# Kernel optimization log

Hardware: AMD Instinct MI355X
Metric: run time of the kernel (lower is better)

## Reference

```python
import jax, jax.numpy as jnp
import numpy as np

N, E, D_IN, D_OUT = 100000, 640000, 128, 128


def setup_inputs() -> dict:
    key = jax.random.key(0)
    ks = jax.random.split(key, 8)
    x = jax.random.normal(ks[0], (N, D_IN), dtype=jnp.float32)
    edge_index = jax.random.randint(ks[1], (2, E), 0, N, dtype=jnp.int64)
    s = 1.0 / np.sqrt(D_IN)
    W_lin = jax.random.uniform(ks[2], (D_IN, D_OUT), jnp.float32, -s, s)
    b_lin = jax.random.uniform(ks[3], (D_OUT,), jnp.float32, -s, s)
    W_st = jax.random.uniform(ks[4], (D_IN, D_OUT), jnp.float32, -s, s)
    b_st = jax.random.uniform(ks[5], (D_OUT,), jnp.float32, -s, s)
    W_ts = jax.random.uniform(ks[6], (D_IN, D_OUT), jnp.float32, -s, s)
    b_ts = jax.random.uniform(ks[7], (D_OUT,), jnp.float32, -s, s)
    return {"x": x, "edge_index": edge_index, "W_lin": W_lin, "b_lin": b_lin,
            "W_st": W_st, "b_st": b_st, "W_ts": W_ts, "b_ts": b_ts}


def _scatter_mean(feat_src, idx_dst, num_nodes):
    # gather-then-segment-sum mean aggregation over variable-degree neighborhoods
    summed = jax.ops.segment_sum(feat_src, idx_dst, num_segments=num_nodes)
    cnt = jax.ops.segment_sum(jnp.ones((feat_src.shape[0],), feat_src.dtype),
                              idx_dst, num_segments=num_nodes)
    return summed / jnp.maximum(cnt, 1.0)[:, None]


def reference(x, edge_index, W_lin, b_lin, W_st, b_st, W_ts, b_ts):
    src, dst = edge_index[0], edge_index[1]
    alpha = 0.5
    # SAGEConv(flow='source_to_target', root_weight=False): mean over in-neighbors (src -> dst)
    agg_st = _scatter_mean(x[src], dst, x.shape[0])
    out_st = agg_st @ W_st + b_st
    # SAGEConv(flow='target_to_source'): mean over out-neighbors (dst -> src)
    agg_ts = _scatter_mean(x[dst], src, x.shape[0])
    out_ts = agg_ts @ W_ts + b_ts
    return x @ W_lin + b_lin + (1.0 - alpha) * out_st + alpha * out_ts
```

## Files before the change

### kernel.cpp

```cpp
#include <hip/hip_runtime.h>

#define D    128
#define BROW 32
#define CAPE 31

typedef short short8 __attribute__((ext_vector_type(8)));
typedef float f32x4  __attribute__((ext_vector_type(4)));

static __device__ __forceinline__ unsigned short f2bf(float f) {
    union { float f; unsigned u; } v; v.f = f;
    unsigned r = v.u + 0x7FFFu + ((v.u >> 16) & 1u);
    return (unsigned short)(r >> 16);
}
static __device__ __forceinline__ float bf2f(unsigned short h) {
    union { unsigned u; float f; } v; v.u = ((unsigned)h) << 16;
    return v.f;
}

#define CH 2048

__global__ __launch_bounds__(256) void k_phase0(
    const float* __restrict__ x, const int* __restrict__ ei,
    const float* __restrict__ W_lin, const float* __restrict__ W_st,
    const float* __restrict__ W_ts,
    unsigned short* __restrict__ xb, unsigned short* __restrict__ wtf,
    int* __restrict__ cnt, int* __restrict__ ent,
    int E, int N, int t8, int nbuild, int ncvt)
{
    int b = blockIdx.x;
    if (b < nbuild) {
        const int part  = b & 7;
        const int chunk = b >> 3;
        const int P  = (2 * N + 7) >> 3;
        const int lo = part * P;
        const int hi = lo + P;
        int gg[16], vv[16], pp[16];
        #pragma unroll
        for (int k = 0; k < 8; ++k) {
            int e = chunk * CH + k * 256 + threadIdx.x;
            int s = -1, d = -1;
            if (e < E) { s = ei[e]; d = ei[E + e]; }
            int gts = N + s;
            gg[2 * k]     = (s >= 0 && d >= lo && d < hi) ? d : -1;
            vv[2 * k]     = s;
            gg[2 * k + 1] = (s >= 0 && gts >= lo && gts < hi) ? gts : -1;
            vv[2 * k + 1] = d;
        }
        #pragma unroll
        for (int k = 0; k < 16; ++k)
            if (gg[k] >= 0) pp[k] = atomicAdd(cnt + gg[k], 1);
        #pragma unroll
        for (int k = 0; k < 16; ++k)
            if (gg[k] >= 0 && pp[k] < CAPE)
                ent[(size_t)gg[k] * BROW + pp[k]] = vv[k];
    } else if (b < nbuild + ncvt) {
        int i = (b - nbuild) * 256 + threadIdx.x;
        if (i >= t8) return;
        const float4* p = (const float4*)(x + (size_t)i * 8);
        float4 a = p[0], c = p[1];
        unsigned r0 = (unsigned)f2bf(a.x) | ((unsigned)f2bf(a.y) << 16);
        unsigned r1 = (unsigned)f2bf(a.z) | ((unsigned)f2bf(a.w) << 16);
        unsigned r2 = (unsigned)f2bf(c.x) | ((unsigned)f2bf(c.y) << 16);
        unsigned r3 = (unsigned)f2bf(c.z) | ((unsigned)f2bf(c.w) << 16);
        *((uint4*)(xb + (size_t)i * 8)) = make_uint4(r0, r1, r2, r3);
    } else {
        int g = (b - nbuild - ncvt) * 256 + threadIdx.x;
        if (g >= 3 * 4 * 8 * 64) return;
        int lane = g & 63;
        int tile = (g >> 6) & 7;
        int ks   = (g >> 9) & 3;
        int m    = g >> 11;
        const float* W = (m == 0) ? W_lin : (m == 1) ? W_st : W_ts;
        float scale = (m == 0) ? 1.0f : 0.5f;
        int n = tile * 16 + (lane & 15);
        int kbase = ks * 32 + (lane >> 4) * 8;
        unsigned short* dst = wtf + (size_t)g * 8;
        #pragma unroll
        for (int j = 0; j < 8; ++j)
            dst[j] = f2bf(W[(size_t)(kbase + j) * D + n] * scale);
    }
}

__global__ __launch_bounds__(256, 5) void k_fused(
    const unsigned short* __restrict__ xb,
    const int* __restrict__ cnt, const int* __restrict__ ent,
    const unsigned short* __restrict__ wtf,
    const float* __restrict__ b_lin, const float* __restrict__ b_st,
    const float* __restrict__ b_ts,
    float* __restrict__ out, int N)
{
    __shared__ unsigned short aggF[2 * 4 * 64 * 4 * 8];

    const int tid  = threadIdx.x;
    const int row0 = blockIdx.x * 64;

    {
        const int grp = tid >> 3;
        const int l8  = tid & 7;
        const int ks  = l8 >> 1;
        const int qd0 = (l8 & 1) * 2;
        const unsigned short* xcol = xb + (l8 << 4);

        int slot0 = grp * 4;
        int gn = row0 + (slot0 & 63); if (gn > N - 1) gn = N - 1;
        size_t g = (size_t)(slot0 >> 6) * N + gn;
        const int* row = ent + g * BROW;
        int4 h = *(const int4*)row;
        int dg = cnt[g];

        for (int s = 0; s < 4; ++s) {
            const int* rowN = row; int4 hn = h; int dgn = dg;
            if (s < 3) {
                int slot1 = grp * 4 + s + 1;
                int gn1 = row0 + (slot1 & 63); if (gn1 > N - 1) gn1 = N - 1;
                size_t g1 = (size_t)(slot1 >> 6) * N + gn1;
                rowN = ent + g1 * BROW;
                hn = *(const int4*)rowN;
                dgn = cnt[g1];
            }
            int slotc = grp * 4 + s;
            int dirc = slotc >> 6, ic = slotc & 63;
            int deg = dg > CAPE ? CAPE : dg;

            float a0[8], a1[8];
            #pragma unroll
            for (int t = 0; t < 8; ++t) { a0[t] = 0.f; a1[t] = 0.f; }

            int j = 0;
            if (deg >= 4) {
                {
                    const unsigned short* r0 = xcol + (size_t)h.x * D;
                    const unsigned short* r1 = xcol + (size_t)h.y * D;
                    const unsigned short* r2 = xcol + (size_t)h.z * D;
                    const unsigned short* r3 = xcol + (size_t)h.w * D;
                    short8 u00 = *(const short8*)r0, u01 = *(const short8*)(r0 + 8);
                    short8 u10 = *(const short8*)r1, u11 = *(const short8*)(r1 + 8);
                    short8 u20 = *(const short8*)r2, u21 = *(const short8*)(r2 + 8);
                    short8 u30 = *(const short8*)r3, u31 = *(const short8*)(r3 + 8);
                    #pragma unroll
                    for (int t = 0; t < 8; ++t) {
                        a0[t] += (bf2f((unsigned short)u00[t]) + bf2f((unsigned short)u10[t]))
                               + (bf2f((unsigned short)u20[t]) + bf2f((unsigned short)u30[t]));
                        a1[t] += (bf2f((unsigned short)u01[t]) + bf2f((unsigned short)u11[t]))
                               + (bf2f((unsigned short)u21[t]) + bf2f((unsigned short)u31[t]));
                    }
                }
                for (j = 4; j + 4 <= deg; j += 4) {
                    const unsigned short* r0 = xcol + (size_t)row[j]     * D;
                    const unsigned short* r1 = xcol + (size_t)row[j + 1] * D;
                    const unsigned short* r2 = xcol + (size_t)row[j + 2] * D;
                    const unsigned short* r3 = xcol + (size_t)row[j + 3] * D;
                    short8 u00 = *(const short8*)r0, u01 = *(const short8*)(r0 + 8);
                    short8 u10 = *(const short8*)r1, u11 = *(const short8*)(r1 + 8);
                    short8 u20 = *(const short8*)r2, u21 = *(const short8*)(r2 + 8);
                    short8 u30 = *(const short8*)r3, u31 = *(const short8*)(r3 + 8);
                    #pragma unroll
                    for (int t = 0; t < 8; ++t) {
                        a0[t] += (bf2f((unsigned short)u00[t]) + bf2f((unsigned short)u10[t]))
                               + (bf2f((unsigned short)u20[t]) + bf2f((unsigned short)u30[t]));
                        a1[t] += (bf2f((unsigned short)u01[t]) + bf2f((unsigned short)u11[t]))
                               + (bf2f((unsigned short)u21[t]) + bf2f((unsigned short)u31[t]));
                    }
                }
            }
            for (; j < deg; ++j) {
                const unsigned short* r = xcol + (size_t)row[j] * D;
                short8 u0 = *(const short8*)r, u1 = *(const short8*)(r + 8);
                #pragma unroll
                for (int t = 0; t < 8; ++t) {
                    a0[t] += bf2f((unsigned short)u0[t]);
                    a1[t] += bf2f((unsigned short)u1[t]);
                }
            }

            float inv = 1.0f / fmaxf((float)deg, 1.0f);
            short8 o0, o1;
            #pragma unroll
            for (int t = 0; t < 8; ++t) {
                o0[t] = (short)f2bf(a0[t] * inv);
                o1[t] = (short)f2bf(a1[t] * inv);
            }
            short8* afp = ((short8*)aggF) + (((dirc * 4 + ks) * 64 + ic) * 4) + qd0;
            afp[0] = o0;
            afp[1] = o1;

            row = rowN; h = hn; dg = dgn;
        }
    }

    const int w    = tid >> 6;
    const int lane = tid & 63;
    const int quad = lane >> 4;
    const int l15  = lane & 15;
    const int wrow = w * 16 + l15;
    int rowA = row0 + wrow; if (rowA > N - 1) rowA = N - 1;

    f32x4 acc[8];
    #pragma unroll
    for (int t = 0; t < 8; ++t) acc[t] = (f32x4){0.f, 0.f, 0.f, 0.f};

    {
        short8 a[4];
        const unsigned short* ap = xb + (size_t)rowA * D + quad * 8;
        #pragma unroll
        for (int ks = 0; ks < 4; ++ks)
            a[ks] = *(const short8*)(ap + ks * 32);
        const short8* bw = (const short8*)wtf;
        #pragma unroll
        for (int ks = 0; ks < 4; ++ks) {
            #pragma unroll
            for (int t = 0; t < 8; ++t) {
                short8 bb = bw[(ks * 8 + t) * 64 + lane];
                acc[t] = __builtin_amdgcn_mfma_f32_16x16x32_bf16(a[ks], bb, acc[t], 0, 0, 0);
            }
        }
    }
    __syncthreads();

    for (int m = 1; m < 3; ++m) {
        short8 a[4];
        const short8* af = (const short8*)aggF;
        #pragma unroll
        for (int ks = 0; ks < 4; ++ks)
            a[ks] = af[(((m - 1) * 4 + ks) << 8) + wrow * 4 + quad];
        const short8* bw = ((const short8*)wtf) + m * 2048;
        #pragma unroll
        for (int ks = 0; ks < 4; ++ks) {
            #pragma unroll
            for (int t = 0; t < 8; ++t) {
                short8 bb = bw[(ks * 8 + t) * 64 + lane];
                acc[t] = __builtin_amdgcn_mfma_f32_16x16x32_bf16(a[ks], bb, acc[t], 0, 0, 0);
            }
        }
    }

    #pragma unroll
    for (int t = 0; t < 8; ++t) {
        int col = t * 16 + l15;
        float bj = b_lin[col] + 0.5f * (b_st[col] + b_ts[col]);
        #pragma unroll
        for (int i = 0; i < 4; ++i) {
            int row = row0 + w * 16 + quad * 4 + i;
            if (row < N)
                __builtin_nontemporal_store(acc[t][i] + bj, &out[(size_t)row * D + col]);
        }
    }
}

extern "C" void kernel_launch(void* const* d_in, const int* in_sizes, int n_in,
                              void* d_out, int out_size, void* d_ws, size_t ws_size,
                              hipStream_t stream)
{
    const float* x     = (const float*)d_in[0];
    const int*   ei    = (const int*)d_in[1];
    const float* W_lin = (const float*)d_in[2];
    const float* b_lin = (const float*)d_in[3];
    const float* W_st  = (const float*)d_in[4];
    const float* b_st  = (const float*)d_in[5];
    const float* W_ts  = (const float*)d_in[6];
    const float* b_ts  = (const float*)d_in[7];
    float*       out   = (float*)d_out;

    const int N = in_sizes[0] / D;
    const int E = in_sizes[1] / 2;
    const int M = 2 * N;

    char* base = (char*)d_ws;
    int* cnt             = (int*)base;            base += (size_t)M * 4;
    int* ent             = (int*)base;            base += (size_t)M * BROW * 4;
    unsigned short* xb   = (unsigned short*)base; base += (size_t)N * D * 2;
    unsigned short* wtf  = (unsigned short*)base; base += 3 * 16384 * 2;

    hipMemsetAsync(cnt, 0, (size_t)M * 4, stream);

    const int t8     = N * D / 8;
    const int nbuild = 8 * ((E + CH - 1) / CH);
    const int ncvt   = (t8 + 255) / 256;
    const int nprep  = 24;

    k_phase0<<<dim3(nbuild + ncvt + nprep), dim3(256), 0, stream>>>(
        x, ei, W_lin, W_st, W_ts, xb, wtf, cnt, ent, E, N, t8, nbuild, ncvt);
    k_fused<<<dim3((N + 63) / 64), dim3(256), 0, stream>>>(
        xb, cnt, ent, wtf, b_lin, b_st, b_ts, out, N);
}
```

Measured before the change: 269.4 us.

## Halve rows per block, widen gather lanes, pad with zero row

Each block now covers 32 rows instead of 64, so the grid doubles and occupancy is raised to 6 waves per SIMD. The gather gives each of 16 lanes 8 columns per neighbor, in place of 8 lanes with 16 columns, and the final MFMA stage is split so each wave computes 4 of the 8 column tiles. A zero row appended to the bf16 copy of x lets the gather loop always fetch four neighbors per step, padding with that row, which removes the scalar remainder loop and branch divergence. The cost is more redundant loads of the weight fragments per block and some wasted loads on the zero row.

```diff
diff --git a/kernel.cpp b/kernel.cpp
--- a/kernel.cpp
+++ b/kernel.cpp
@@ -55,7 +55,11 @@
                 ent[(size_t)gg[k] * BROW + pp[k]] = vv[k];
     } else if (b < nbuild + ncvt) {
         int i = (b - nbuild) * 256 + threadIdx.x;
-        if (i >= t8) return;
+        if (i >= t8 + D / 8) return;
+        if (i >= t8) {
+            *((uint4*)(xb + (size_t)i * 8)) = make_uint4(0, 0, 0, 0);
+            return;
+        }
         const float4* p = (const float4*)(x + (size_t)i * 8);
         float4 a = p[0], c = p[1];
         unsigned r0 = (unsigned)f2bf(a.x) | ((unsigned)f2bf(a.y) << 16);
@@ -81,7 +85,7 @@
     }
 }
 
-__global__ __launch_bounds__(256, 5) void k_fused(
+__global__ __launch_bounds__(256, 6) void k_fused(
     const unsigned short* __restrict__ xb,
     const int* __restrict__ cnt, const int* __restrict__ ent,
     const unsigned short* __restrict__ wtf,
@@ -89,21 +93,19 @@
     const float* __restrict__ b_ts,
     float* __restrict__ out, int N)
 {
-    __shared__ unsigned short aggF[2 * 4 * 64 * 4 * 8];
+    __shared__ unsigned short aggF[2 * 4 * 32 * 4 * 8];
 
     const int tid  = threadIdx.x;
-    const int row0 = blockIdx.x * 64;
+    const int row0 = blockIdx.x * 32;
 
     {
-        const int grp = tid >> 3;
-        const int l8  = tid & 7;
-        const int ks  = l8 >> 1;
-        const int qd0 = (l8 & 1) * 2;
-        const unsigned short* xcol = xb + (l8 << 4);
+        const int grp = tid >> 4;
+        const int l16 = tid & 15;
+        const unsigned short* xcol = xb + (l16 << 3);
 
         int slot0 = grp * 4;
-        int gn = row0 + (slot0 & 63); if (gn > N - 1) gn = N - 1;
-        size_t g = (size_t)(slot0 >> 6) * N + gn;
+        int gn = row0 + (slot0 & 31); if (gn > N - 1) gn = N - 1;
+        size_t g = (size_t)(slot0 >> 5) * N + gn;
         const int* row = ent + g * BROW;
         int4 h = *(const int4*)row;
         int dg = cnt[g];
@@ -112,92 +114,74 @@
             const int* rowN = row; int4 hn = h; int dgn = dg;
             if (s < 3) {
                 int slot1 = grp * 4 + s + 1;
-                int gn1 = row0 + (slot1 & 63); if (gn1 > N - 1) gn1 = N - 1;
-                size_t g1 = (size_t)(slot1 >> 6) * N + gn1;
+                int gn1 = row0 + (slot1 & 31); if (gn1 > N - 1) gn1 = N - 1;
+                size_t g1 = (size_t)(slot1 >> 5) * N + gn1;
                 rowN = ent + g1 * BROW;
                 hn = *(const int4*)rowN;
                 dgn = cnt[g1];
             }
             int slotc = grp * 4 + s;
-            int dirc = slotc >> 6, ic = slotc & 63;
+            int dirc = slotc >> 5, ic = slotc & 31;
             int deg = dg > CAPE ? CAPE : dg;
-
-            float a0[8], a1[8];
-            #pragma unroll
-            for (int t = 0; t < 8; ++t) { a0[t] = 0.f; a1[t] = 0.f; }
-
-            int j = 0;
-            if (deg >= 4) {
-                {
-                    const unsigned short* r0 = xcol + (size_t)h.x * D;
-                    const unsigned short* r1 = xcol + (size_t)h.y * D;
-                    const unsigned short* r2 = xcol + (size_t)h.z * D;
-                    const unsigned short* r3 = xcol + (size_t)h.w * D;
-                    short8 u00 = *(const short8*)r0, u01 = *(const short8*)(r0 + 8);
-                    short8 u10 = *(const short8*)r1, u11 = *(const short8*)(r1 + 8);
-                    short8 u20 = *(const short8*)r2, u21 = *(const short8*)(r2 + 8);
-                    short8 u30 = *(const short8*)r3, u31 = *(const short8*)(r3 + 8);
+            int R = (deg + 3) >> 2;
+
+            float a[8];
+            #pragma unroll
+            for (int t = 0; t < 8; ++t) a[t] = 0.f;
+
+            if (R > 0) {
+                int n0 = h.x;
+                int n1 = (1 < deg) ? h.y : N;
+                int n2 = (2 < deg) ? h.z : N;
+                int n3 = (3 < deg) ? h.w : N;
+                short8 u0 = *(const short8*)(xcol + (size_t)n0 * D);
+                short8 u1 = *(const short8*)(xcol + (size_t)n1 * D);
+                short8 u2 = *(const short8*)(xcol + (size_t)n2 * D);
+                short8 u3 = *(const short8*)(xcol + (size_t)n3 * D);
+                for (int r = 1; r < R; ++r) {
+                    int j = r * 4;
+                    int m0 = row[j];
+                    int m1 = (j + 1 < deg) ? row[j + 1] : N;
+                    int m2 = (j + 2 < deg) ? row[j + 2] : N;
+                    int m3 = (j + 3 < deg) ? row[j + 3] : N;
+                    short8 v0 = *(const short8*)(xcol + (size_t)m0 * D);
+                    short8 v1 = *(const short8*)(xcol + (size_t)m1 * D);
+                    short8 v2 = *(const short8*)(xcol + (size_t)m2 * D);
+                    short8 v3 = *(const short8*)(xcol + (size_t)m3 * D);
                     #pragma unroll
-                    for (int t = 0; t < 8; ++t) {
-                        a0[t] += (bf2f((unsigned short)u00[t]) + bf2f((unsigned short)u10[t]))
-                               + (bf2f((unsigned short)u20[t]) + bf2f((unsigned short)u30[t]));
-                        a1[t] += (bf2f((unsigned short)u01[t]) + bf2f((unsigned short)u11[t]))
-                               + (bf2f((unsigned short)u21[t]) + bf2f((unsigned short)u31[t]));
-                    }
+                    for (int t = 0; t < 8; ++t)
+                        a[t] += (bf2f((unsigned short)u0[t]) + bf2f((unsigned short)u1[t]))
+                              + (bf2f((unsigned short)u2[t]) + bf2f((unsigned short)u3[t]));
+                    u0 = v0; u1 = v1; u2 = v2; u3 = v3;
                 }
-                for (j = 4; j + 4 <= deg; j += 4) {
-                    const unsigned short* r0 = xcol + (size_t)row[j]     * D;
-                    const unsigned short* r1 = xcol + (size_t)row[j + 1] * D;
-                    const unsigned short* r2 = xcol + (size_t)row[j + 2] * D;
-                    const unsigned short* r3 = xcol + (size_t)row[j + 3] * D;
-                    short8 u00 = *(const short8*)r0, u01 = *(const short8*)(r0 + 8);
-                    short8 u10 = *(const short8*)r1, u11 = *(const short8*)(r1 + 8);
-                    short8 u20 = *(const short8*)r2, u21 = *(const short8*)(r2 + 8);
-                    short8 u30 = *(const short8*)r3, u31 = *(const short8*)(r3 + 8);
-                    #pragma unroll
-                    for (int t = 0; t < 8; ++t) {
-                        a0[t] += (bf2f((unsigned short)u00[t]) + bf2f((unsigned short)u10[t]))
-                               + (bf2f((unsigned short)u20[t]) + bf2f((unsigned short)u30[t]));
-                        a1[t] += (bf2f((unsigned short)u01[t]) + bf2f((unsigned short)u11[t]))
-                               + (bf2f((unsigned short)u21[t]) + bf2f((unsigned short)u31[t]));
-                    }
-                }
-            }
-            for (; j < deg; ++j) {
-                const unsigned short* r = xcol + (size_t)row[j] * D;
-                short8 u0 = *(const short8*)r, u1 = *(const short8*)(r + 8);
                 #pragma unroll
-                for (int t = 0; t < 8; ++t) {
-                    a0[t] += bf2f((unsigned short)u0[t]);
-                    a1[t] += bf2f((unsigned short)u1[t]);
-                }
+                for (int t = 0; t < 8; ++t)
+                    a[t] += (bf2f((unsigned short)u0[t]) + bf2f((unsigned short)u1[t]))
+                          + (bf2f((unsigned short)u2[t]) + bf2f((unsigned short)u3[t]));
             }
 
             float inv = 1.0f / fmaxf((float)deg, 1.0f);
-            short8 o0, o1;
-            #pragma unroll
-            for (int t = 0; t < 8; ++t) {
-                o0[t] = (short)f2bf(a0[t] * inv);
-                o1[t] = (short)f2bf(a1[t] * inv);
-            }
-            short8* afp = ((short8*)aggF) + (((dirc * 4 + ks) * 64 + ic) * 4) + qd0;
-            afp[0] = o0;
-            afp[1] = o1;
+            short8 o;
+            #pragma unroll
+            for (int t = 0; t < 8; ++t) o[t] = (short)f2bf(a[t] * inv);
+            ((short8*)aggF)[((dirc * 4 + (l16 >> 2)) * 32 + ic) * 4 + (l16 & 3)] = o;
 
             row = rowN; h = hn; dg = dgn;
         }
     }
 
-    const int w    = tid >> 6;
-    const int lane = tid & 63;
-    const int quad = lane >> 4;
-    const int l15  = lane & 15;
-    const int wrow = w * 16 + l15;
+    const int w     = tid >> 6;
+    const int lane  = tid & 63;
+    const int quad  = lane >> 4;
+    const int l15   = lane & 15;
+    const int rhalf = w & 1;
+    const int tb    = (w >> 1) * 4;
+    const int wrow  = rhalf * 16 + l15;
     int rowA = row0 + wrow; if (rowA > N - 1) rowA = N - 1;
 
-    f32x4 acc[8];
+    f32x4 acc[4];
     #pragma unroll
-    for (int t = 0; t < 8; ++t) acc[t] = (f32x4){0.f, 0.f, 0.f, 0.f};
+    for (int t = 0; t < 4; ++t) acc[t] = (f32x4){0.f, 0.f, 0.f, 0.f};
 
     {
         short8 a[4];
@@ -209,8 +193,8 @@
         #pragma unroll
         for (int ks = 0; ks < 4; ++ks) {
             #pragma unroll
-            for (int t = 0; t < 8; ++t) {
-                short8 bb = bw[(ks * 8 + t) * 64 + lane];
+            for (int t = 0; t < 4; ++t) {
+                short8 bb = bw[(ks * 8 + tb + t) * 64 + lane];
                 acc[t] = __builtin_amdgcn_mfma_f32_16x16x32_bf16(a[ks], bb, acc[t], 0, 0, 0);
             }
         }
@@ -222,25 +206,25 @@
         const short8* af = (const short8*)aggF;
         #pragma unroll
         for (int ks = 0; ks < 4; ++ks)
-            a[ks] = af[(((m - 1) * 4 + ks) << 8) + wrow * 4 + quad];
+            a[ks] = af[((m - 1) * 4 + ks) * 128 + wrow * 4 + quad];
         const short8* bw = ((const short8*)wtf) + m * 2048;
         #pragma unroll
         for (int ks = 0; ks < 4; ++ks) {
             #pragma unroll
-            for (int t = 0; t < 8; ++t) {
-                short8 bb = bw[(ks * 8 + t) * 64 + lane];
+            for (int t = 0; t < 4; ++t) {
+                short8 bb = bw[(ks * 8 + tb + t) * 64 + lane];
                 acc[t] = __builtin_amdgcn_mfma_f32_16x16x32_bf16(a[ks], bb, acc[t], 0, 0, 0);
             }
         }
     }
 
     #pragma unroll
-    for (int t = 0; t < 8; ++t) {
-        int col = t * 16 + l15;
+    for (int t = 0; t < 4; ++t) {
+        int col = (tb + t) * 16 + l15;
         float bj = b_lin[col] + 0.5f * (b_st[col] + b_ts[col]);
         #pragma unroll
         for (int i = 0; i < 4; ++i) {
-            int row = row0 + w * 16 + quad * 4 + i;
+            int row = row0 + rhalf * 16 + quad * 4 + i;
             if (row < N)
                 __builtin_nontemporal_store(acc[t][i] + bj, &out[(size_t)row * D + col]);
         }
@@ -268,18 +252,18 @@
     char* base = (char*)d_ws;
     int* cnt             = (int*)base;            base += (size_t)M * 4;
     int* ent             = (int*)base;            base += (size_t)M * BROW * 4;
-    unsigned short* xb   = (unsigned short*)base; base += (size_t)N * D * 2;
+    unsigned short* xb   = (unsigned short*)base; base += (size_t)(N + 1) * D * 2;
     unsigned short* wtf  = (unsigned short*)base; base += 3 * 16384 * 2;
 
     hipMemsetAsync(cnt, 0, (size_t)M * 4, stream);
 
     const int t8     = N * D / 8;
     const int nbuild = 8 * ((E + CH - 1) / CH);
-    const int ncvt   = (t8 + 255) / 256;
+    const int ncvt   = (t8 + D / 8 + 255) / 256;
     const int nprep  = 24;
 
     k_phase0<<<dim3(nbuild + ncvt + nprep), dim3(256), 0, stream>>>(
         x, ei, W_lin, W_st, W_ts, xb, wtf, cnt, ent, E, N, t8, nbuild, ncvt);
-    k_fused<<<dim3((N + 63) / 64), dim3(256), 0, stream>>>(
+    k_fused<<<dim3((N + 31) / 32), dim3(256), 0, stream>>>(
         xb, cnt, ent, wtf, b_lin, b_st, b_ts, out, N);
 }
```

Result: faster. 247.6 us (-8.1%).
